# Kernel optimization log

Hardware: AMD Instinct MI355X
Metric: run time of the kernel (lower is better)

## Reference

```python
import jax, jax.numpy as jnp
import numpy as np

GRID_SIZE = 64
K = 3
GRID_RANGE = (-1.0, 1.0)
NUM_BASIS = GRID_SIZE + K


def _knots():
    # extended knot vector: k repeats of the left end, uniform grid, k repeats of the right end
    g = jnp.linspace(GRID_RANGE[0], GRID_RANGE[1], GRID_SIZE + 1, dtype=jnp.float32)
    left = jnp.full((K,), GRID_RANGE[0], dtype=jnp.float32)
    right = jnp.full((K,), GRID_RANGE[1], dtype=jnp.float32)
    return jnp.concatenate([left, g, right])  # (GRID_SIZE + 2K + 1,)


def reference(x):
    """Cox-de Boor B-spline basis, bottom-up DP (vectorized over batch).

    x: (B,) float32 -> (B, NUM_BASIS) float32
    """
    knots = _knots()
    n0 = GRID_SIZE + 2 * K  # number of degree-0 basis functions
    xb = x[:, None]  # (B, 1)
    # degree 0: indicator of half-open interval [t_i, t_{i+1})
    N = ((xb >= knots[None, :n0]) & (xb < knots[None, 1:n0 + 1])).astype(x.dtype)
    for d in range(1, K + 1):
        n = n0 - d  # number of degree-d bases
        t_i = knots[:n]
        t_id = knots[d:d + n]
        t_i1 = knots[1:1 + n]
        t_id1 = knots[d + 1:d + 1 + n]
        den1 = t_id - t_i
        den2 = t_id1 - t_i1
        # term is dropped entirely when the denominator is zero (repeated knots)
        w1 = jnp.where(den1 != 0, (xb - t_i) / jnp.where(den1 != 0, den1, 1.0), 0.0)
        w2 = jnp.where(den2 != 0, (t_id1 - xb) / jnp.where(den2 != 0, den2, 1.0), 0.0)
        N = w1 * N[:, :n] + w2 * N[:, 1:n + 1]
    return N  # (B, NUM_BASIS)


def setup_inputs() -> dict:
    key = jax.random.key(0)
    x = jax.random.uniform(key, (2_000_000,), minval=-1.0, maxval=1.0, dtype=jnp.float32)
    return {"x": x}
```

## Files before the change

kernel.cpp:

```cpp
#include <hip/hip_runtime.h>

#define ROWS_PER_BLOCK 128
#define NUM_BASIS 67
#define TILE_FLOATS (ROWS_PER_BLOCK * NUM_BASIS)
#define TILE_VEC4 (TILE_FLOATS / 4)

__device__ __forceinline__ float kv(int i) {
    i = min(max(i, 3), 67);
    return (float)(i - 35) * 0.03125f;
}

__global__ __launch_bounds__(256) void SplineBasis_kernel(const float* __restrict__ x,
                                                          float* __restrict__ out,
                                                          int B) {
    __shared__ __align__(16) float tile[TILE_FLOATS];
    const int tid = threadIdx.x;
    const int blockRow0 = blockIdx.x * ROWS_PER_BLOCK;

    float4* t4 = (float4*)tile;
    for (int i = tid; i < TILE_VEC4; i += 256) t4[i] = make_float4(0.f, 0.f, 0.f, 0.f);
    __syncthreads();

    if (tid < ROWS_PER_BLOCK) {
        const int row = blockRow0 + tid;
        if (row < B) {
            const float xv = x[row];
            if (xv >= -1.0f && xv < 1.0f) {
                int cell = (int)floorf((xv + 1.0f) * 32.0f);
                cell = min(max(cell, 0), 63);
                int m = cell + 3;
                while (m > 3 && xv < kv(m)) --m;
                while (m < 66 && xv >= kv(m + 1)) ++m;

                float N[4], left[4], right[4];
                N[0] = 1.0f;
#pragma unroll
                for (int d = 1; d <= 3; ++d) {
                    left[d]  = xv - kv(m + 1 - d);
                    right[d] = kv(m + d) - xv;
                    float saved = 0.0f;
#pragma unroll
                    for (int r = 0; r < d; ++r) {
                        float temp = N[r] / (right[r + 1] + left[d - r]);
                        N[r] = saved + right[r + 1] * temp;
                        saved = left[d - r] * temp;
                    }
                    N[d] = saved;
                }

                const int c0 = tid * NUM_BASIS + (m - 3);
                tile[c0 + 0] = N[0];
                tile[c0 + 1] = N[1];
                tile[c0 + 2] = N[2];
                tile[c0 + 3] = N[3];
            }
        }
    }
    __syncthreads();

    const int rows = min(ROWS_PER_BLOCK, B - blockRow0);
    if (rows == ROWS_PER_BLOCK) {
        float4* o4 = (float4*)(out + (size_t)blockRow0 * NUM_BASIS);
        for (int i = tid; i < TILE_VEC4; i += 256) o4[i] = t4[i];
    } else if (rows > 0) {
        const int n = rows * NUM_BASIS;
        float* o = out + (size_t)blockRow0 * NUM_BASIS;
        for (int i = tid; i < n; i += 256) o[i] = tile[i];
    }
}

extern "C" void kernel_launch(void* const* d_in, const int* in_sizes, int n_in,
                              void* d_out, int out_size, void* d_ws, size_t ws_size,
                              hipStream_t stream) {
    const float* x = (const float*)d_in[0];
    float* out = (float*)d_out;
    const int B = in_sizes[0];
    const int nblocks = (B + ROWS_PER_BLOCK - 1) / ROWS_PER_BLOCK;
    SplineBasis_kernel<<<nblocks, 256, 0, stream>>>(x, out, B);
}
```

Measured before the change: 519.1 us.

## Use persistent blocks looping over tiles with incremental zeroing and x prefetch

```diff
diff --git a/kernel.cpp b/kernel.cpp
--- a/kernel.cpp
+++ b/kernel.cpp
@@ -1,31 +1,68 @@
 #include <hip/hip_runtime.h>
 
-#define ROWS_PER_BLOCK 128
+#define ROWS 128
 #define NUM_BASIS 67
-#define TILE_FLOATS (ROWS_PER_BLOCK * NUM_BASIS)
-#define TILE_VEC4 (TILE_FLOATS / 4)
+#define TILE_FLOATS (ROWS * NUM_BASIS)
+#define TILE_V4 (TILE_FLOATS / 4)
+#define NBLOCKS 1024
+#define NTHREADS 256
 
 __device__ __forceinline__ float kv(int i) {
     i = min(max(i, 3), 67);
     return (float)(i - 35) * 0.03125f;
 }
 
-__global__ __launch_bounds__(256) void SplineBasis_kernel(const float* __restrict__ x,
-                                                          float* __restrict__ out,
-                                                          int B) {
+__device__ __forceinline__ void lgkm_barrier() {
+    asm volatile("s_waitcnt lgkmcnt(0)" ::: "memory");
+    __builtin_amdgcn_s_barrier();
+    asm volatile("" ::: "memory");
+}
+
+__global__ __launch_bounds__(NTHREADS) void SplineBasis_kernel(const float* __restrict__ x,
+                                                               float* __restrict__ out,
+                                                               int B) {
     __shared__ __align__(16) float tile[TILE_FLOATS];
     const int tid = threadIdx.x;
-    const int blockRow0 = blockIdx.x * ROWS_PER_BLOCK;
+
+    const int ntiles = (B + ROWS - 1) / ROWS;
+    const int q = ntiles / NBLOCKS, r = ntiles % NBLOCKS;
+    const int bid = (int)blockIdx.x;
+    const int myn = q + (bid < r ? 1 : 0);
+    const int t0 = bid * q + min(bid, r);
+    if (myn == 0) return;
 
     float4* t4 = (float4*)tile;
-    for (int i = tid; i < TILE_VEC4; i += 256) t4[i] = make_float4(0.f, 0.f, 0.f, 0.f);
-    __syncthreads();
+    for (int i = tid; i < TILE_V4; i += NTHREADS) t4[i] = make_float4(0.f, 0.f, 0.f, 0.f);
 
-    if (tid < ROWS_PER_BLOCK) {
-        const int row = blockRow0 + tid;
-        if (row < B) {
-            const float xv = x[row];
-            if (xv >= -1.0f && xv < 1.0f) {
+    float xv = 0.0f;
+    bool havex = false;
+    if (tid < ROWS) {
+        const int row = t0 * ROWS + tid;
+        if (row < B) { xv = x[row]; havex = true; }
+    }
+
+    int prev_c0 = -1;
+
+    for (int t = 0; t < myn; ++t) {
+        const int tile_idx = t0 + t;
+
+        lgkm_barrier();
+
+        if (tid < ROWS) {
+            float xnext = 0.0f;
+            bool havenext = false;
+            if (t + 1 < myn) {
+                const int row = (tile_idx + 1) * ROWS + tid;
+                if (row < B) { xnext = x[row]; havenext = true; }
+            }
+
+            if (prev_c0 >= 0) {
+                tile[prev_c0 + 0] = 0.f; tile[prev_c0 + 1] = 0.f;
+                tile[prev_c0 + 2] = 0.f; tile[prev_c0 + 3] = 0.f;
+                prev_c0 = -1;
+            }
+
+            if (havex && xv >= -1.0f && xv < 1.0f) {
                 int cell = (int)floorf((xv + 1.0f) * 32.0f);
                 cell = min(max(cell, 0), 63);
                 int m = cell + 3;
@@ -40,10 +77,10 @@
                     right[d] = kv(m + d) - xv;
                     float saved = 0.0f;
 #pragma unroll
-                    for (int r = 0; r < d; ++r) {
-                        float temp = N[r] / (right[r + 1] + left[d - r]);
-                        N[r] = saved + right[r + 1] * temp;
-                        saved = left[d - r] * temp;
+                    for (int rr = 0; rr < d; ++rr) {
+                        float temp = N[rr] / (right[rr + 1] + left[d - rr]);
+                        N[rr] = saved + right[rr + 1] * temp;
+                        saved = left[d - rr] * temp;
                     }
                     N[d] = saved;
                 }
@@ -53,19 +90,22 @@
                 tile[c0 + 1] = N[1];
                 tile[c0 + 2] = N[2];
                 tile[c0 + 3] = N[3];
+                prev_c0 = c0;
             }
+            xv = xnext; havex = havenext;
         }
-    }
-    __syncthreads();
 
-    const int rows = min(ROWS_PER_BLOCK, B - blockRow0);
-    if (rows == ROWS_PER_BLOCK) {
-        float4* o4 = (float4*)(out + (size_t)blockRow0 * NUM_BASIS);
-        for (int i = tid; i < TILE_VEC4; i += 256) o4[i] = t4[i];
-    } else if (rows > 0) {
-        const int n = rows * NUM_BASIS;
-        float* o = out + (size_t)blockRow0 * NUM_BASIS;
-        for (int i = tid; i < n; i += 256) o[i] = tile[i];
+        lgkm_barrier();
+
+        const int rows = min(ROWS, B - tile_idx * ROWS);
+        if (rows == ROWS) {
+            float4* o4 = (float4*)(out + (size_t)tile_idx * TILE_FLOATS);
+            for (int i = tid; i < TILE_V4; i += NTHREADS) o4[i] = t4[i];
+        } else if (rows > 0) {
+            const int n = rows * NUM_BASIS;
+            float* o = out + (size_t)tile_idx * TILE_FLOATS;
+            for (int i = tid; i < n; i += NTHREADS) o[i] = tile[i];
+        }
     }
 }
 
@@ -75,6 +115,7 @@
     const float* x = (const float*)d_in[0];
     float* out = (float*)d_out;
     const int B = in_sizes[0];
-    const int nblocks = (B + ROWS_PER_BLOCK - 1) / ROWS_PER_BLOCK;
-    SplineBasis_kernel<<<nblocks, 256, 0, stream>>>(x, out, B);
+    const int ntiles = (B + ROWS - 1) / ROWS;
+    const int nblocks = ntiles < NBLOCKS ? ntiles : NBLOCKS;
+    SplineBasis_kernel<<<nblocks, NTHREADS, 0, stream>>>(x, out, B);
 }
```

Result: slower. 533.2 us (+2.7%).

## Replace shared-memory tile with memset plus sparse scatter of nonzero basis values

Applied to the files above, without the earlier changes.

```diff
diff --git a/kernel.cpp b/kernel.cpp
--- a/kernel.cpp
+++ b/kernel.cpp
@@ -1,72 +1,49 @@
 #include <hip/hip_runtime.h>
 
-#define ROWS_PER_BLOCK 128
 #define NUM_BASIS 67
-#define TILE_FLOATS (ROWS_PER_BLOCK * NUM_BASIS)
-#define TILE_VEC4 (TILE_FLOATS / 4)
+#define NTHREADS 256
 
 __device__ __forceinline__ float kv(int i) {
     i = min(max(i, 3), 67);
     return (float)(i - 35) * 0.03125f;
 }
 
-__global__ __launch_bounds__(256) void SplineBasis_kernel(const float* __restrict__ x,
-                                                          float* __restrict__ out,
-                                                          int B) {
-    __shared__ __align__(16) float tile[TILE_FLOATS];
-    const int tid = threadIdx.x;
-    const int blockRow0 = blockIdx.x * ROWS_PER_BLOCK;
+__global__ __launch_bounds__(NTHREADS) void SplineBasis_scatter(const float* __restrict__ x,
+                                                                float* __restrict__ out,
+                                                                int B) {
+    const int row = blockIdx.x * NTHREADS + threadIdx.x;
+    if (row >= B) return;
 
-    float4* t4 = (float4*)tile;
-    for (int i = tid; i < TILE_VEC4; i += 256) t4[i] = make_float4(0.f, 0.f, 0.f, 0.f);
-    __syncthreads();
+    const float xv = x[row];
+    if (!(xv >= -1.0f && xv < 1.0f)) return;
 
-    if (tid < ROWS_PER_BLOCK) {
-        const int row = blockRow0 + tid;
-        if (row < B) {
-            const float xv = x[row];
-            if (xv >= -1.0f && xv < 1.0f) {
-                int cell = (int)floorf((xv + 1.0f) * 32.0f);
-                cell = min(max(cell, 0), 63);
-                int m = cell + 3;
-                while (m > 3 && xv < kv(m)) --m;
-                while (m < 66 && xv >= kv(m + 1)) ++m;
+    int cell = (int)floorf((xv + 1.0f) * 32.0f);
+    cell = min(max(cell, 0), 63);
+    int m = cell + 3;
+    while (m > 3 && xv < kv(m)) --m;
+    while (m < 66 && xv >= kv(m + 1)) ++m;
 
-                float N[4], left[4], right[4];
-                N[0] = 1.0f;
+    float N[4], left[4], right[4];
+    N[0] = 1.0f;
 #pragma unroll
-                for (int d = 1; d <= 3; ++d) {
-                    left[d]  = xv - kv(m + 1 - d);
-                    right[d] = kv(m + d) - xv;
-                    float saved = 0.0f;
+    for (int d = 1; d <= 3; ++d) {
+        left[d]  = xv - kv(m + 1 - d);
+        right[d] = kv(m + d) - xv;
+        float saved = 0.0f;
 #pragma unroll
-                    for (int r = 0; r < d; ++r) {
-                        float temp = N[r] / (right[r + 1] + left[d - r]);
-                        N[r] = saved + right[r + 1] * temp;
-                        saved = left[d - r] * temp;
-                    }
-                    N[d] = saved;
-                }
+        for (int r = 0; r < d; ++r) {
+            float temp = N[r] / (right[r + 1] + left[d - r]);
+            N[r] = saved + right[r + 1] * temp;
+            saved = left[d - r] * temp;
+        }
+        N[d] = saved;
+    }
 
-                const int c0 = tid * NUM_BASIS + (m - 3);
-                tile[c0 + 0] = N[0];
-                tile[c0 + 1] = N[1];
-                tile[c0 + 2] = N[2];
-                tile[c0 + 3] = N[3];
-            }
-        }
-    }
-    __syncthreads();
-
-    const int rows = min(ROWS_PER_BLOCK, B - blockRow0);
-    if (rows == ROWS_PER_BLOCK) {
-        float4* o4 = (float4*)(out + (size_t)blockRow0 * NUM_BASIS);
-        for (int i = tid; i < TILE_VEC4; i += 256) o4[i] = t4[i];
-    } else if (rows > 0) {
-        const int n = rows * NUM_BASIS;
-        float* o = out + (size_t)blockRow0 * NUM_BASIS;
-        for (int i = tid; i < n; i += 256) o[i] = tile[i];
-    }
+    float* o = out + (size_t)row * NUM_BASIS + (m - 3);
+    o[0] = N[0];
+    o[1] = N[1];
+    o[2] = N[2];
+    o[3] = N[3];
 }
 
 extern "C" void kernel_launch(void* const* d_in, const int* in_sizes, int n_in,
@@ -75,6 +52,9 @@
     const float* x = (const float*)d_in[0];
     float* out = (float*)d_out;
     const int B = in_sizes[0];
-    const int nblocks = (B + ROWS_PER_BLOCK - 1) / ROWS_PER_BLOCK;
-    SplineBasis_kernel<<<nblocks, 256, 0, stream>>>(x, out, B);
+
+    hipMemsetAsync(out, 0, (size_t)B * NUM_BASIS * sizeof(float), stream);
+
+    const int nblocks = (B + NTHREADS - 1) / NTHREADS;
+    SplineBasis_scatter<<<nblocks, NTHREADS, 0, stream>>>(x, out, B);
 }
```

New measurement: 635.4 us. 1.22x slower.
